# Kernel optimization log

Measured on AMD Instinct MI355X. Metric: run time of the kernel, lower is better.

Reference implementation:

```python
import jax, jax.numpy as jnp
import numpy as np

EPS_NORM = 1e-12   # F.normalize default eps
EPS_COS = 1e-8     # F.cosine_similarity default eps
NUM_LAYERS = 3


def _l2norm(x, eps=EPS_NORM):
    n = jnp.sqrt(jnp.sum(x * x, axis=-1, keepdims=True))
    return x / jnp.maximum(n, eps)


def setup_inputs() -> dict:
    key = jax.random.key(0)
    ks = jax.random.split(key, 16)
    NU, NI, D, E = 200000, 100000, 64, 1000000
    NA, NB, H, F = 20000, 30000, 32, 8
    return {
        "user_emb_w": jax.random.normal(ks[0], (NU, D), jnp.float32) * 0.1,
        "artist_emb_w": jax.random.normal(ks[1], (NA, D), jnp.float32) * 0.1,
        "album_emb_w": jax.random.normal(ks[2], (NB, D), jnp.float32) * 0.1,
        "item_audio": jax.random.normal(ks[3], (NI, D), jnp.float32),
        "adapter_W": jax.random.normal(ks[4], (D, D), jnp.float32) * (1.0 / np.sqrt(D)),
        "adapter_b": jnp.zeros((D,), jnp.float32),
        "mlp_W1": jax.random.normal(ks[5], (H, F), jnp.float32) * (1.0 / np.sqrt(F)),
        "mlp_b1": jnp.zeros((H,), jnp.float32),
        "mlp_W2": jax.random.normal(ks[6], (1, H), jnp.float32) * (1.0 / np.sqrt(H)),
        "mlp_b2": jnp.zeros((1,), jnp.float32),
        "edge_features": jax.random.normal(ks[7], (2 * E, F), jnp.float32),
        "edge_user": jax.random.randint(ks[8], (E,), 0, NU, jnp.int32),
        "edge_item": jax.random.randint(ks[9], (E,), 0, NI, jnp.int32),
        "artist_ids": jax.random.randint(ks[10], (NI,), 0, NA, jnp.int32),
        "album_ids": jax.random.randint(ks[11], (NI,), 0, NB, jnp.int32),
        "user_idx": jax.random.randint(ks[12], (4096,), 0, NU, jnp.int32),
        "pos_item_id": jax.random.randint(ks[13], (4096,), 0, NI, jnp.int32),
    }


def reference(user_emb_w, artist_emb_w, album_emb_w, item_audio,
              adapter_W, adapter_b, mlp_W1, mlp_b1, mlp_W2, mlp_b2,
              edge_features, edge_user, edge_item, artist_ids, album_ids,
              user_idx, pos_item_id):
    NU = user_emb_w.shape[0]
    NI = item_audio.shape[0]
    N = NU + NI

    # EdgeWeightMLP: sigmoid(W2 @ relu(W1 @ f + b1) + b2), per edge -> [2E]
    h = jax.nn.relu(edge_features @ mlp_W1.T + mlp_b1)
    w = jax.nn.sigmoid(h @ mlp_W2.T + mlp_b2)[:, 0]

    # item embedding fusion + AudioAdapter (Linear + L2 normalize)
    item_embed = item_audio + artist_emb_w[artist_ids] + album_emb_w[album_ids]
    item_embed = _l2norm(item_embed @ adapter_W.T + adapter_b)

    x = jnp.concatenate([user_emb_w, item_embed], axis=0)  # [N, D]

    # symmetric edge list in global node ids (items offset by NU)
    item_g = edge_item + NU
    row = jnp.concatenate([edge_user, item_g])   # source
    col = jnp.concatenate([item_g, edge_user])   # target

    # LGConv gcn_norm (no self loops): deg over targets with edge weights
    deg = jax.ops.segment_sum(w, col, num_segments=N)
    dis = jnp.where(deg > 0, jax.lax.rsqrt(jnp.where(deg > 0, deg, 1.0)), 0.0)
    norm_e = dis[row] * w * dis[col]  # [2E]

    for _ in range(NUM_LAYERS):
        msgs = x[row] * norm_e[:, None]              # [2E, D] gather + scale
        x = jax.ops.segment_sum(msgs, col, num_segments=N)  # scatter-add

    x = _l2norm(x)

    u_emb = x[user_idx]                # [B, D]
    pos_emb = x[NU + pos_item_id]      # [B, D]

    # cosine similarity alignment loss (F.cosine_similarity, eps=1e-8)
    un = jnp.sqrt(jnp.sum(u_emb * u_emb, axis=-1))
    pn = jnp.sqrt(jnp.sum(pos_emb * pos_emb, axis=-1))
    cos = jnp.sum(u_emb * pos_emb, axis=-1) / (jnp.maximum(un, EPS_COS) * jnp.maximum(pn, EPS_COS))
    align_loss = jnp.mean(1.0 - cos)

    return u_emb, align_loss
```

## Files before the change

kernel.cpp:

```cpp
#include <hip/hip_runtime.h>
#include <math.h>

#define NU 200000
#define NI 100000
#define NN 300000
#define DD 64
#define EDGES 1000000
#define E2 2000000
#define BATCH 4096
#define SCAN_CHUNK 1024
#define NBLK1 ((NN + SCAN_CHUNK - 1) / SCAN_CHUNK)
#define FIX_SCALE 131072.0f
#define FIX_INV   7.62939453125e-06f

#define MLP_BLOCKS2 ((E2 + 511) / 512)
#define FUSE_BLOCKS4 (NI / 16)
#define COPY_BLOCKS (NU * DD / 4 / 256)
#define PREP_PERIODS 2084
#define PREP_GRID (PREP_PERIODS * 11)

__device__ __forceinline__ unsigned short f2bf(float f) {
    unsigned u = __float_as_uint(f);
    return (unsigned short)((u + 0x7fffu + ((u >> 16) & 1u)) >> 16);
}
__device__ __forceinline__ float bflo(unsigned v) { return __uint_as_float(v << 16); }
__device__ __forceinline__ float bfhi(unsigned v) { return __uint_as_float(v & 0xffff0000u); }

__global__ __launch_bounds__(256) void k_prep(
    const float* __restrict__ ef, const float* __restrict__ W1,
    const float* __restrict__ b1, const float* __restrict__ W2,
    const float* __restrict__ b2, const int* __restrict__ eu,
    const int* __restrict__ ei, float* __restrict__ w,
    unsigned* __restrict__ degc, int* __restrict__ epos,
    const float* __restrict__ item_audio, const float* __restrict__ artist_emb,
    const float* __restrict__ album_emb, const int* __restrict__ artist_ids,
    const int* __restrict__ album_ids, const float* __restrict__ aW,
    const float* __restrict__ ab, const float* __restrict__ user_emb,
    unsigned short* __restrict__ x) {
    __shared__ float4 sW4[64][16];
    __shared__ float4 sv4[16][16];
    __shared__ float4 sW1v[64];
    __shared__ float sb1[32], sW2s[32], sb2v;
    int bid = blockIdx.x;
    int tid = threadIdx.x;
    int r = bid % 11, base = bid / 11;
    if (r < 2) {
        int ablk = base * 2 + r;
        if (ablk >= MLP_BLOCKS2) return;
        if (tid < 64) sW1v[tid] = ((const float4*)W1)[tid];
        else if (tid < 96) sb1[tid - 64] = b1[tid - 64];
        else if (tid < 128) sW2s[tid - 96] = W2[tid - 96];
        else if (tid == 128) sb2v = b2[0];
        __syncthreads();
        int e0 = ablk * 512 + tid;
        int e1 = e0 + 256;
        int e0c = e0 < E2 ? e0 : 0;
        int e1c = e1 < E2 ? e1 : 0;
        int c0 = (e0c < EDGES) ? (NU + ei[e0c]) : eu[e0c - EDGES];
        int c1 = (e1c < EDGES) ? (NU + ei[e1c]) : eu[e1c - EDGES];
        float4 fa0 = ((const float4*)ef)[2 * e0c];
        float4 fa1 = ((const float4*)ef)[2 * e0c + 1];
        float4 fb0 = ((const float4*)ef)[2 * e1c];
        float4 fb1 = ((const float4*)ef)[2 * e1c + 1];
        float z0 = sb2v, z1 = sb2v;
#pragma unroll 8
        for (int i = 0; i < 32; ++i) {
            float4 wa = sW1v[2 * i], wb = sW1v[2 * i + 1];
            float bi = sb1[i], wo = sW2s[i];
            float a0 = bi + fa0.x * wa.x + fa0.y * wa.y + fa0.z * wa.z +
                       fa0.w * wa.w + fa1.x * wb.x + fa1.y * wb.y +
                       fa1.z * wb.z + fa1.w * wb.w;
            float a1 = bi + fb0.x * wa.x + fb0.y * wa.y + fb0.z * wa.z +
                       fb0.w * wa.w + fb1.x * wb.x + fb1.y * wb.y +
                       fb1.z * wb.z + fb1.w * wb.w;
            z0 += wo * fmaxf(a0, 0.0f);
            z1 += wo * fmaxf(a1, 0.0f);
        }
        if (e0 < E2) {
            float we = 1.0f / (1.0f + __expf(-z0));
            w[e0] = we;
            unsigned old = atomicAdd(
                &degc[c0], (1u << 24) | (unsigned)(we * FIX_SCALE + 0.5f));
            epos[e0] = (int)(old >> 24);
        }
        if (e1 < E2) {
            float we = 1.0f / (1.0f + __expf(-z1));
            w[e1] = we;
            unsigned old = atomicAdd(
                &degc[c1], (1u << 24) | (unsigned)(we * FIX_SCALE + 0.5f));
            epos[e1] = (int)(old >> 24);
        }
        return;
    }
    if (r <= 4) {
        int j = base * 3 + (r - 2);
        if (j >= FUSE_BLOCKS4) return;
#pragma unroll
        for (int s = 0; s < 4; ++s) {
            int i4 = tid + s * 256;
            int row = i4 >> 4, c4 = i4 & 15;
            sW4[row][(c4 & 8) | ((c4 ^ row) & 7)] = ((const float4*)aW)[i4];
        }
        __syncthreads();
        int wave = tid >> 6, lane = tid & 63;
        int it0 = j * 16 + wave * 4;
        float* svf = (float*)sv4;
#pragma unroll
        for (int t = 0; t < 4; ++t) {
            int it = it0 + t;
            int ar = artist_ids[it], al = album_ids[it];
            float v = item_audio[it * DD + lane] + artist_emb[ar * DD + lane] +
                      album_emb[al * DD + lane];
            svf[(wave * 4 + t) * DD + lane] = v;
        }
        float bias = ab[lane];
        float t0 = bias, t1 = bias, t2 = bias, t3 = bias;
#pragma unroll
        for (int k4 = 0; k4 < 16; ++k4) {
            float4 wv = sW4[lane][(k4 & 8) | ((k4 ^ lane) & 7)];
            float4 va = sv4[wave * 4 + 0][k4];
            float4 vb = sv4[wave * 4 + 1][k4];
            float4 vc = sv4[wave * 4 + 2][k4];
            float4 vd = sv4[wave * 4 + 3][k4];
            t0 += wv.x * va.x + wv.y * va.y + wv.z * va.z + wv.w * va.w;
            t1 += wv.x * vb.x + wv.y * vb.y + wv.z * vb.z + wv.w * vb.w;
            t2 += wv.x * vc.x + wv.y * vc.y + wv.z * vc.z + wv.w * vc.w;
            t3 += wv.x * vd.x + wv.y * vd.y + wv.z * vd.z + wv.w * vd.w;
        }
        float s0 = t0 * t0, s1 = t1 * t1, s2 = t2 * t2, s3 = t3 * t3;
        for (int m = 32; m >= 1; m >>= 1) {
            s0 += __shfl_xor(s0, m, 64);
            s1 += __shfl_xor(s1, m, 64);
            s2 += __shfl_xor(s2, m, 64);
            s3 += __shfl_xor(s3, m, 64);
        }
        x[(NU + it0 + 0) * DD + lane] = f2bf(t0 / fmaxf(sqrtf(s0), 1e-12f));
        x[(NU + it0 + 1) * DD + lane] = f2bf(t1 / fmaxf(sqrtf(s1), 1e-12f));
        x[(NU + it0 + 2) * DD + lane] = f2bf(t2 / fmaxf(sqrtf(s2), 1e-12f));
        x[(NU + it0 + 3) * DD + lane] = f2bf(t3 / fmaxf(sqrtf(s3), 1e-12f));
        return;
    }
    int cb = base * 6 + (r - 5);
    if (cb >= COPY_BLOCKS) return;
    int i = cb * 256 + tid;
    float4 v = ((const float4*)user_emb)[i];
    ushort4 o;
    o.x = f2bf(v.x); o.y = f2bf(v.y); o.z = f2bf(v.z); o.w = f2bf(v.w);
    ((ushort4*)x)[i] = o;
}

__global__ __launch_bounds__(1024) void k_scan_local(
    const unsigned* __restrict__ degc, int* __restrict__ rowptr,
    int* __restrict__ bsum) {
    __shared__ int sh[SCAN_CHUNK];
    int tid = threadIdx.x;
    int i = blockIdx.x * SCAN_CHUNK + tid;
    int cnt = (i < NN) ? (int)(degc[i] >> 24) : 0;
    int v = (cnt + 7) & ~7;
    sh[tid] = v;
    __syncthreads();
    for (int off = 1; off < SCAN_CHUNK; off <<= 1) {
        int t = (tid >= off) ? sh[tid - off] : 0;
        __syncthreads();
        sh[tid] += t;
        __syncthreads();
    }
    if (i < NN) rowptr[i] = sh[tid] - v;
    if (tid == SCAN_CHUNK - 1) bsum[blockIdx.x] = sh[tid];
}

__global__ __launch_bounds__(512) void k_scan_bsum(int* __restrict__ bsum) {
    __shared__ int sh[512];
    int tid = threadIdx.x;
    int v = (tid < NBLK1) ? bsum[tid] : 0;
    sh[tid] = v;
    __syncthreads();
    for (int off = 1; off < 512; off <<= 1) {
        int t = (tid >= off) ? sh[tid - off] : 0;
        __syncthreads();
        sh[tid] += t;
        __syncthreads();
    }
    if (tid < NBLK1) bsum[tid] = sh[tid] - v;
}

__global__ void k_scan_add_dis(int* __restrict__ rowptr, const int* __restrict__ bsum,
                               const unsigned* __restrict__ degc,
                               float* __restrict__ dis, int2* __restrict__ csre) {
    int i = blockIdx.x * blockDim.x + threadIdx.x;
    if (i >= NN) return;
    int rp = rowptr[i] + bsum[i >> 10];
    rowptr[i] = rp;
    unsigned dc = degc[i];
    int cnt = (int)(dc >> 24);
    int pcnt = (cnt + 7) & ~7;
    float d = (float)(dc & 0xFFFFFFu) * FIX_INV;
    dis[i] = d > 0.0f ? rsqrtf(d) : 0.0f;
    for (int k = cnt; k < pcnt; ++k) csre[rp + k] = make_int2(0, 0);
    if (i == NN - 1) rowptr[NN] = rp + pcnt;
}

__global__ void k_fill(const float* __restrict__ w, const int* __restrict__ eu,
                       const int* __restrict__ ei, const float* __restrict__ dis,
                       const int* __restrict__ rowptr, const int* __restrict__ epos,
                       int2* __restrict__ csre) {
    int e = blockIdx.x * blockDim.x + threadIdx.x;
    if (e >= E2) return;
    int r, c;
    if (e < EDGES) { r = eu[e]; c = NU + ei[e]; }
    else           { r = NU + ei[e - EDGES]; c = eu[e - EDGES]; }
    int pos = rowptr[c] + epos[e];
    csre[pos] = make_int2(r * (DD * 2), __float_as_int(dis[r] * w[e] * dis[c]));
}

__global__ void k_mark(const int* __restrict__ uidx, const int* __restrict__ pidx,
                       const int* __restrict__ rowptr, const int2* __restrict__ csre,
                       unsigned char* __restrict__ flags) {
    int t = blockIdx.x * blockDim.x + threadIdx.x;
    if (t >= 2 * BATCH) return;
    int row = (t < BATCH) ? uidx[t] : NU + pidx[t - BATCH];
    int beg = rowptr[row], end = rowptr[row + 1];
    for (int e = beg; e < end; ++e) flags[((unsigned)csre[e].x) >> 7] = 1;
}

__device__ __forceinline__ void pull4(const char* __restrict__ xb,
                                      const int2* __restrict__ csre,
                                      int beg, int end, int q2, int t8,
                                      float& a0, float& a1, float& a2, float& a3) {
    a0 = a1 = a2 = a3 = 0.0f;
    for (int e = beg; e < end; e += 8) {
        int4 s = *(const int4*)(csre + (e + q2));
        uint2 va = *(const uint2*)(xb + (unsigned)s.x + t8);
        uint2 vb = *(const uint2*)(xb + (unsigned)s.z + t8);
        float wa = __int_as_float(s.y), wb = __int_as_float(s.w);
        a0 = fmaf(bflo(va.x), wa, a0);
        a1 = fmaf(bfhi(va.x), wa, a1);
        a2 = fmaf(bflo(va.y), wa, a2);
        a3 = fmaf(bfhi(va.y), wa, a3);
        a0 = fmaf(bflo(vb.x), wb, a0);
        a1 = fmaf(bfhi(vb.x), wb, a1);
        a2 = fmaf(bflo(vb.y), wb, a2);
        a3 = fmaf(bfhi(vb.y), wb, a3);
    }
    a0 += __shfl_xor(a0, 16, 64); a1 += __shfl_xor(a1, 16, 64);
    a2 += __shfl_xor(a2, 16, 64); a3 += __shfl_xor(a3, 16, 64);
    a0 += __shfl_xor(a0, 32, 64); a1 += __shfl_xor(a1, 32, 64);
    a2 += __shfl_xor(a2, 32, 64); a3 += __shfl_xor(a3, 32, 64);
}

template <bool FLAGS>
__global__ __launch_bounds__(256) void k_prop(
    const unsigned short* __restrict__ x, const int* __restrict__ rowptr,
    const int2* __restrict__ csre, unsigned short* __restrict__ xn,
    const unsigned char* __restrict__ flags) {
    int tid = threadIdx.x;
    int node = blockIdx.x * 4 + (tid >> 6);
    if (node >= NN) return;
    if (FLAGS && !flags[node]) return;
    int lane = tid & 63;
    int q2 = (lane >> 4) << 1;
    int t8 = (lane & 15) * 8;
    float a0, a1, a2, a3;
    pull4((const char*)x, csre, rowptr[node], rowptr[node + 1], q2, t8,
          a0, a1, a2, a3);
    if ((lane >> 4) == 0) {
        unsigned lo = ((unsigned)f2bf(a1) << 16) | (unsigned)f2bf(a0);
        unsigned hi = ((unsigned)f2bf(a3) << 16) | (unsigned)f2bf(a2);
        *(uint2*)((char*)xn + (size_t)node * 128 + t8) = make_uint2(lo, hi);
    }
}

__global__ __launch_bounds__(256) void k_tail(
    const unsigned short* __restrict__ x, const int* __restrict__ rowptr,
    const int2* __restrict__ csre, const int* __restrict__ uidx,
    const int* __restrict__ pidx, float* __restrict__ out) {
    int tid = threadIdx.x;
    int b = blockIdx.x * 4 + (tid >> 6);
    if (b >= BATCH) return;
    int lane = tid & 63;
    int q2 = (lane >> 4) << 1;
    int t8 = (lane & 15) * 8;
    const char* xb = (const char*)x;
    int un = uidx[b], pn = NU + pidx[b];
    float u0, u1, u2, u3, p0, p1, p2, p3, ss, s;
    pull4(xb, csre, rowptr[un], rowptr[un + 1], q2, t8, u0, u1, u2, u3);
    ss = u0 * u0 + u1 * u1 + u2 * u2 + u3 * u3;
    for (int m = 8; m >= 1; m >>= 1) ss += __shfl_xor(ss, m, 64);
    s = 1.0f / fmaxf(sqrtf(ss), 1e-12f);
    u0 *= s; u1 *= s; u2 *= s; u3 *= s;
    pull4(xb, csre, rowptr[pn], rowptr[pn + 1], q2, t8, p0, p1, p2, p3);
    ss = p0 * p0 + p1 * p1 + p2 * p2 + p3 * p3;
    for (int m = 8; m >= 1; m >>= 1) ss += __shfl_xor(ss, m, 64);
    s = 1.0f / fmaxf(sqrtf(ss), 1e-12f);
    p0 *= s; p1 *= s; p2 *= s; p3 *= s;
    if ((lane >> 4) == 0)
        ((float4*)out)[b * 16 + (t8 >> 3)] = make_float4(u0, u1, u2, u3);
    float dot = u0 * p0 + u1 * p1 + u2 * p2 + u3 * p3;
    float uu = u0 * u0 + u1 * u1 + u2 * u2 + u3 * u3;
    float pp = p0 * p0 + p1 * p1 + p2 * p2 + p3 * p3;
    for (int m = 8; m >= 1; m >>= 1) {
        dot += __shfl_xor(dot, m, 64);
        uu  += __shfl_xor(uu, m, 64);
        pp  += __shfl_xor(pp, m, 64);
    }
    if (lane == 0) {
        float cs = dot / (fmaxf(sqrtf(uu), 1e-8f) * fmaxf(sqrtf(pp), 1e-8f));
        atomicAdd(out + BATCH * DD, (1.0f - cs) * (1.0f / BATCH));
    }
}

extern "C" void kernel_launch(void* const* d_in, const int* in_sizes, int n_in,
                              void* d_out, int out_size, void* d_ws, size_t ws_size,
                              hipStream_t stream) {
    const float* user_emb      = (const float*)d_in[0];
    const float* artist_emb    = (const float*)d_in[1];
    const float* album_emb     = (const float*)d_in[2];
    const float* item_audio    = (const float*)d_in[3];
    const float* adapter_W     = (const float*)d_in[4];
    const float* adapter_b     = (const float*)d_in[5];
    const float* mlp_W1        = (const float*)d_in[6];
    const float* mlp_b1        = (const float*)d_in[7];
    const float* mlp_W2        = (const float*)d_in[8];
    const float* mlp_b2        = (const float*)d_in[9];
    const float* edge_features = (const float*)d_in[10];
    const int*   edge_user     = (const int*)d_in[11];
    const int*   edge_item     = (const int*)d_in[12];
    const int*   artist_ids    = (const int*)d_in[13];
    const int*   album_ids     = (const int*)d_in[14];
    const int*   user_idx      = (const int*)d_in[15];
    const int*   pos_item_id   = (const int*)d_in[16];

    char* p = (char*)d_ws;
    unsigned short* XB0 = (unsigned short*)p; p += (size_t)NN * DD * 2;
    unsigned short* XB1 = (unsigned short*)p; p += (size_t)NN * DD * 2;
    float* W       = (float*)p; p += (size_t)E2 * 4;
    int2*  CSRE    = (int2*)p;  p += (size_t)4200000 * 8;
    int*   EPOS    = (int*)p;   p += (size_t)E2 * 4;
    unsigned* DEGC = (unsigned*)p; p += (size_t)NN * 8;
    float* DIS     = (float*)p; p += (size_t)NN * 4;
    int*   ROWPTR  = (int*)p;   p += (size_t)(NN + 1) * 4;
    int*   BSUM    = (int*)p;   p += (size_t)((NBLK1 + 3) & ~3) * 4;
    unsigned char* FLAGS = (unsigned char*)p; p += (size_t)NN;

    hipMemsetAsync(DEGC, 0, NN * sizeof(unsigned), stream);
    hipMemsetAsync(FLAGS, 0, NN, stream);
    hipMemsetAsync((float*)d_out + BATCH * DD, 0, sizeof(float), stream);

    k_prep<<<PREP_GRID, 256, 0, stream>>>(
        edge_features, mlp_W1, mlp_b1, mlp_W2, mlp_b2, edge_user, edge_item,
        W, DEGC, EPOS, item_audio, artist_emb, album_emb, artist_ids, album_ids,
        adapter_W, adapter_b, user_emb, XB0);

    k_scan_local<<<NBLK1, SCAN_CHUNK, 0, stream>>>(DEGC, ROWPTR, BSUM);
    k_scan_bsum<<<1, 512, 0, stream>>>(BSUM);
    k_scan_add_dis<<<(NN + 255) / 256, 256, 0, stream>>>(ROWPTR, BSUM, DEGC, DIS,
                                                         CSRE);
    k_fill<<<(E2 + 255) / 256, 256, 0, stream>>>(W, edge_user, edge_item, DIS,
                                                 ROWPTR, EPOS, CSRE);
    k_mark<<<(2 * BATCH + 255) / 256, 256, 0, stream>>>(user_idx, pos_item_id,
                                                        ROWPTR, CSRE, FLAGS);

    k_prop<false><<<(NN + 3) / 4, 256, 0, stream>>>(XB0, ROWPTR, CSRE, XB1, nullptr);
    k_prop<true><<<(NN + 3) / 4, 256, 0, stream>>>(XB1, ROWPTR, CSRE, XB0, FLAGS);

    k_tail<<<BATCH / 4, 256, 0, stream>>>(XB0, ROWPTR, CSRE, user_idx,
                                          pos_item_id, (float*)d_out);
}
```

Before: 345.1 us.

## Drop CSR padding, factor target norm out of edges, use 16-byte row gathers

Removes the pad-to-8 rows from the CSR edge array and the zero-fill that went with them. The gather loop now bounds-checks each edge slot against the row end instead. The target-side rsqrt degree factor is moved out of each stored edge weight and applied once per node after the reduction; the tail kernel can skip it because L2 normalisation cancels it. The gather is reorganised so 8 lane groups each fetch one edge's 16-byte slice instead of 4 groups fetching two 8-byte slices, trading a per-edge predicate for a smaller edge array and wider loads.

```diff
diff --git a/kernel.cpp b/kernel.cpp
--- a/kernel.cpp
+++ b/kernel.cpp
@@ -155,8 +155,7 @@
     __shared__ int sh[SCAN_CHUNK];
     int tid = threadIdx.x;
     int i = blockIdx.x * SCAN_CHUNK + tid;
-    int cnt = (i < NN) ? (int)(degc[i] >> 24) : 0;
-    int v = (cnt + 7) & ~7;
+    int v = (i < NN) ? (int)(degc[i] >> 24) : 0;
     sh[tid] = v;
     __syncthreads();
     for (int off = 1; off < SCAN_CHUNK; off <<= 1) {
@@ -186,18 +185,15 @@
 
 __global__ void k_scan_add_dis(int* __restrict__ rowptr, const int* __restrict__ bsum,
                                const unsigned* __restrict__ degc,
-                               float* __restrict__ dis, int2* __restrict__ csre) {
+                               float* __restrict__ dis) {
     int i = blockIdx.x * blockDim.x + threadIdx.x;
     if (i >= NN) return;
     int rp = rowptr[i] + bsum[i >> 10];
     rowptr[i] = rp;
     unsigned dc = degc[i];
-    int cnt = (int)(dc >> 24);
-    int pcnt = (cnt + 7) & ~7;
     float d = (float)(dc & 0xFFFFFFu) * FIX_INV;
     dis[i] = d > 0.0f ? rsqrtf(d) : 0.0f;
-    for (int k = cnt; k < pcnt; ++k) csre[rp + k] = make_int2(0, 0);
-    if (i == NN - 1) rowptr[NN] = rp + pcnt;
+    if (i == NN - 1) rowptr[NN] = rp + (int)(dc >> 24);
 }
 
 __global__ void k_fill(const float* __restrict__ w, const int* __restrict__ eu,
@@ -210,7 +206,7 @@
     if (e < EDGES) { r = eu[e]; c = NU + ei[e]; }
     else           { r = NU + ei[e - EDGES]; c = eu[e - EDGES]; }
     int pos = rowptr[c] + epos[e];
-    csre[pos] = make_int2(r * (DD * 2), __float_as_int(dis[r] * w[e] * dis[c]));
+    csre[pos] = make_int2(r * (DD * 2), __float_as_int(dis[r] * w[e]));
 }
 
 __global__ void k_mark(const int* __restrict__ uidx, const int* __restrict__ pidx,
@@ -223,50 +219,53 @@
     for (int e = beg; e < end; ++e) flags[((unsigned)csre[e].x) >> 7] = 1;
 }
 
-__device__ __forceinline__ void pull4(const char* __restrict__ xb,
+__device__ __forceinline__ void pull8(const char* __restrict__ xb,
                                       const int2* __restrict__ csre,
-                                      int beg, int end, int q2, int t8,
-                                      float& a0, float& a1, float& a2, float& a3) {
-    a0 = a1 = a2 = a3 = 0.0f;
+                                      int beg, int end, int g, int t16,
+                                      float (&a)[8]) {
     for (int e = beg; e < end; e += 8) {
-        int4 s = *(const int4*)(csre + (e + q2));
-        uint2 va = *(const uint2*)(xb + (unsigned)s.x + t8);
-        uint2 vb = *(const uint2*)(xb + (unsigned)s.z + t8);
-        float wa = __int_as_float(s.y), wb = __int_as_float(s.w);
-        a0 = fmaf(bflo(va.x), wa, a0);
-        a1 = fmaf(bfhi(va.x), wa, a1);
-        a2 = fmaf(bflo(va.y), wa, a2);
-        a3 = fmaf(bfhi(va.y), wa, a3);
-        a0 = fmaf(bflo(vb.x), wb, a0);
-        a1 = fmaf(bfhi(vb.x), wb, a1);
-        a2 = fmaf(bflo(vb.y), wb, a2);
-        a3 = fmaf(bfhi(vb.y), wb, a3);
-    }
-    a0 += __shfl_xor(a0, 16, 64); a1 += __shfl_xor(a1, 16, 64);
-    a2 += __shfl_xor(a2, 16, 64); a3 += __shfl_xor(a3, 16, 64);
-    a0 += __shfl_xor(a0, 32, 64); a1 += __shfl_xor(a1, 32, 64);
-    a2 += __shfl_xor(a2, 32, 64); a3 += __shfl_xor(a3, 32, 64);
+        int idx = e + g;
+        int2 s = (idx < end) ? csre[idx] : make_int2(0, 0);
+        uint4 v = *(const uint4*)(xb + (unsigned)s.x + t16);
+        float wgt = __int_as_float(s.y);
+        a[0] = fmaf(bflo(v.x), wgt, a[0]);
+        a[1] = fmaf(bfhi(v.x), wgt, a[1]);
+        a[2] = fmaf(bflo(v.y), wgt, a[2]);
+        a[3] = fmaf(bfhi(v.y), wgt, a[3]);
+        a[4] = fmaf(bflo(v.z), wgt, a[4]);
+        a[5] = fmaf(bfhi(v.z), wgt, a[5]);
+        a[6] = fmaf(bflo(v.w), wgt, a[6]);
+        a[7] = fmaf(bfhi(v.w), wgt, a[7]);
+    }
+#pragma unroll
+    for (int m = 8; m <= 32; m <<= 1) {
+#pragma unroll
+        for (int i = 0; i < 8; ++i) a[i] += __shfl_xor(a[i], m, 64);
+    }
 }
 
 template <bool FLAGS>
 __global__ __launch_bounds__(256) void k_prop(
     const unsigned short* __restrict__ x, const int* __restrict__ rowptr,
-    const int2* __restrict__ csre, unsigned short* __restrict__ xn,
-    const unsigned char* __restrict__ flags) {
+    const int2* __restrict__ csre, const float* __restrict__ dis,
+    unsigned short* __restrict__ xn, const unsigned char* __restrict__ flags) {
     int tid = threadIdx.x;
     int node = blockIdx.x * 4 + (tid >> 6);
     if (node >= NN) return;
     if (FLAGS && !flags[node]) return;
     int lane = tid & 63;
-    int q2 = (lane >> 4) << 1;
-    int t8 = (lane & 15) * 8;
-    float a0, a1, a2, a3;
-    pull4((const char*)x, csre, rowptr[node], rowptr[node + 1], q2, t8,
-          a0, a1, a2, a3);
-    if ((lane >> 4) == 0) {
-        unsigned lo = ((unsigned)f2bf(a1) << 16) | (unsigned)f2bf(a0);
-        unsigned hi = ((unsigned)f2bf(a3) << 16) | (unsigned)f2bf(a2);
-        *(uint2*)((char*)xn + (size_t)node * 128 + t8) = make_uint2(lo, hi);
+    int g = lane >> 3;
+    int t16 = (lane & 7) * 16;
+    float a[8] = {0, 0, 0, 0, 0, 0, 0, 0};
+    pull8((const char*)x, csre, rowptr[node], rowptr[node + 1], g, t16, a);
+    float d = dis[node];
+    if (g == 0) {
+        unsigned o0 = ((unsigned)f2bf(a[1] * d) << 16) | (unsigned)f2bf(a[0] * d);
+        unsigned o1 = ((unsigned)f2bf(a[3] * d) << 16) | (unsigned)f2bf(a[2] * d);
+        unsigned o2 = ((unsigned)f2bf(a[5] * d) << 16) | (unsigned)f2bf(a[4] * d);
+        unsigned o3 = ((unsigned)f2bf(a[7] * d) << 16) | (unsigned)f2bf(a[6] * d);
+        *(uint4*)((char*)xn + (size_t)node * 128 + t16) =
+            make_uint4(o0, o1, o2, o3);
     }
 }
 
@@ -278,27 +277,46 @@
     int b = blockIdx.x * 4 + (tid >> 6);
     if (b >= BATCH) return;
     int lane = tid & 63;
-    int q2 = (lane >> 4) << 1;
-    int t8 = (lane & 15) * 8;
+    int g = lane >> 3;
+    int t16 = (lane & 7) * 16;
     const char* xb = (const char*)x;
     int un = uidx[b], pn = NU + pidx[b];
-    float u0, u1, u2, u3, p0, p1, p2, p3, ss, s;
-    pull4(xb, csre, rowptr[un], rowptr[un + 1], q2, t8, u0, u1, u2, u3);
-    ss = u0 * u0 + u1 * u1 + u2 * u2 + u3 * u3;
-    for (int m = 8; m >= 1; m >>= 1) ss += __shfl_xor(ss, m, 64);
+    float u[8] = {0, 0, 0, 0, 0, 0, 0, 0};
+    pull8(xb, csre, rowptr[un], rowptr[un + 1], g, t16, u);
+    float ss = 0.0f;
+#pragma unroll
+    for (int i = 0; i < 8; ++i) ss += u[i] * u[i];
+    ss += __shfl_xor(ss, 1, 64);
+    ss += __shfl_xor(ss, 2, 64);
+    ss += __shfl_xor(ss, 4, 64);
+    float s = 1.0f / fmaxf(sqrtf(ss), 1e-12f);
+#pragma unroll
+    for (int i = 0; i < 8; ++i) u[i] *= s;
+    float p[8] = {0, 0, 0, 0, 0, 0, 0, 0};
+    pull8(xb, csre, rowptr[pn], rowptr[pn + 1], g, t16, p);
+    ss = 0.0f;
+#pragma unroll
+    for (int i = 0; i < 8; ++i) ss += p[i] * p[i];
+    ss += __shfl_xor(ss, 1, 64);
+    ss += __shfl_xor(ss, 2, 64);
+    ss += __shfl_xor(ss, 4, 64);
     s = 1.0f / fmaxf(sqrtf(ss), 1e-12f);
-    u0 *= s; u1 *= s; u2 *= s; u3 *= s;
-    pull4(xb, csre, rowptr[pn], rowptr[pn + 1], q2, t8, p0, p1, p2, p3);
-    ss = p0 * p0 + p1 * p1 + p2 * p2 + p3 * p3;
-    for (int m = 8; m >= 1; m >>= 1) ss += __shfl_xor(ss, m, 64);
-    s = 1.0f / fmaxf(sqrtf(ss), 1e-12f);
-    p0 *= s; p1 *= s; p2 *= s; p3 *= s;
-    if ((lane >> 4) == 0)
-        ((float4*)out)[b * 16 + (t8 >> 3)] = make_float4(u0, u1, u2, u3);
-    float dot = u0 * p0 + u1 * p1 + u2 * p2 + u3 * p3;
-    float uu = u0 * u0 + u1 * u1 + u2 * u2 + u3 * u3;
-    float pp = p0 * p0 + p1 * p1 + p2 * p2 + p3 * p3;
-    for (int m = 8; m >= 1; m >>= 1) {
+#pragma unroll
+    for (int i = 0; i < 8; ++i) p[i] *= s;
+    if (g == 0) {
+        int f4 = b * 16 + (lane & 7) * 2;
+        ((float4*)out)[f4]     = make_float4(u[0], u[1], u[2], u[3]);
+        ((float4*)out)[f4 + 1] = make_float4(u[4], u[5], u[6], u[7]);
+    }
+    float dot = 0.0f, uu = 0.0f, pp = 0.0f;
+#pragma unroll
+    for (int i = 0; i < 8; ++i) {
+        dot += u[i] * p[i];
+        uu += u[i] * u[i];
+        pp += p[i] * p[i];
+    }
+#pragma unroll
+    for (int m = 1; m <= 4; m <<= 1) {
         dot += __shfl_xor(dot, m, 64);
         uu  += __shfl_xor(uu, m, 64);
         pp  += __shfl_xor(pp, m, 64);
@@ -353,15 +371,16 @@
 
     k_scan_local<<<NBLK1, SCAN_CHUNK, 0, stream>>>(DEGC, ROWPTR, BSUM);
     k_scan_bsum<<<1, 512, 0, stream>>>(BSUM);
-    k_scan_add_dis<<<(NN + 255) / 256, 256, 0, stream>>>(ROWPTR, BSUM, DEGC, DIS,
-                                                         CSRE);
+    k_scan_add_dis<<<(NN + 255) / 256, 256, 0, stream>>>(ROWPTR, BSUM, DEGC, DIS);
     k_fill<<<(E2 + 255) / 256, 256, 0, stream>>>(W, edge_user, edge_item, DIS,
                                                  ROWPTR, EPOS, CSRE);
     k_mark<<<(2 * BATCH + 255) / 256, 256, 0, stream>>>(user_idx, pos_item_id,
                                                         ROWPTR, CSRE, FLAGS);
 
-    k_prop<false><<<(NN + 3) / 4, 256, 0, stream>>>(XB0, ROWPTR, CSRE, XB1, nullptr);
-    k_prop<true><<<(NN + 3) / 4, 256, 0, stream>>>(XB1, ROWPTR, CSRE, XB0, FLAGS);
+    k_prop<false><<<(NN + 3) / 4, 256, 0, stream>>>(XB0, ROWPTR, CSRE, DIS, XB1,
+                                                    nullptr);
+    k_prop<true><<<(NN + 3) / 4, 256, 0, stream>>>(XB1, ROWPTR, CSRE, DIS, XB0,
+                                                   FLAGS);
 
     k_tail<<<BATCH / 4, 256, 0, stream>>>(XB0, ROWPTR, CSRE, user_idx,
                                           pos_item_id, (float*)d_out);
```

After: 355.7 us. 3.0% more time.

## Replace three-pass scan with atomic-cursor allocation and fuse marking into propagation

Applied to the files above, without the earlier changes.

The three-kernel prefix scan over padded node degrees becomes a single kernel. Each 1024-node block scans locally and claims its CSR base offset with one atomicAdd on a global cursor, so row segments no longer sit in node order. Row ends now come from the degree count instead of rowptr[node+1], and the target-side dis factor moves out of each edge weight into a per-node scale at output. That scale is a positive constant per row, so it does not change the final L2-normalised tail result. The flag-marking kernel is folded into extra blocks of the first propagation launch, cutting the launch count and the serialised tiny kernels at the cost of a nondeterministic CSR layout.

```diff
diff --git a/kernel.cpp b/kernel.cpp
--- a/kernel.cpp
+++ b/kernel.cpp
@@ -18,6 +18,8 @@
 #define COPY_BLOCKS (NU * DD / 4 / 256)
 #define PREP_PERIODS 2084
 #define PREP_GRID (PREP_PERIODS * 11)
+#define PROP_BLOCKS ((NN + 3) / 4)
+#define MARK_BLOCKS ((2 * BATCH + 255) / 256)
 
 __device__ __forceinline__ unsigned short f2bf(float f) {
     unsigned u = __float_as_uint(f);
@@ -149,13 +151,16 @@
     ((ushort4*)x)[i] = o;
 }
 
-__global__ __launch_bounds__(1024) void k_scan_local(
+__global__ __launch_bounds__(1024) void k_alloc(
     const unsigned* __restrict__ degc, int* __restrict__ rowptr,
-    int* __restrict__ bsum) {
+    float* __restrict__ dis, int2* __restrict__ csre,
+    unsigned* __restrict__ cursor) {
     __shared__ int sh[SCAN_CHUNK];
+    __shared__ int sbase;
     int tid = threadIdx.x;
     int i = blockIdx.x * SCAN_CHUNK + tid;
-    int cnt = (i < NN) ? (int)(degc[i] >> 24) : 0;
+    unsigned dc = (i < NN) ? degc[i] : 0u;
+    int cnt = (int)(dc >> 24);
     int v = (cnt + 7) & ~7;
     sh[tid] = v;
     __syncthreads();
@@ -165,39 +170,16 @@
         sh[tid] += t;
         __syncthreads();
     }
-    if (i < NN) rowptr[i] = sh[tid] - v;
-    if (tid == SCAN_CHUNK - 1) bsum[blockIdx.x] = sh[tid];
-}
-
-__global__ __launch_bounds__(512) void k_scan_bsum(int* __restrict__ bsum) {
-    __shared__ int sh[512];
-    int tid = threadIdx.x;
-    int v = (tid < NBLK1) ? bsum[tid] : 0;
-    sh[tid] = v;
+    if (tid == SCAN_CHUNK - 1)
+        sbase = (int)atomicAdd(cursor, (unsigned)sh[tid]);
     __syncthreads();
-    for (int off = 1; off < 512; off <<= 1) {
-        int t = (tid >= off) ? sh[tid - off] : 0;
-        __syncthreads();
-        sh[tid] += t;
-        __syncthreads();
-    }
-    if (tid < NBLK1) bsum[tid] = sh[tid] - v;
-}
-
-__global__ void k_scan_add_dis(int* __restrict__ rowptr, const int* __restrict__ bsum,
-                               const unsigned* __restrict__ degc,
-                               float* __restrict__ dis, int2* __restrict__ csre) {
-    int i = blockIdx.x * blockDim.x + threadIdx.x;
-    if (i >= NN) return;
-    int rp = rowptr[i] + bsum[i >> 10];
-    rowptr[i] = rp;
-    unsigned dc = degc[i];
-    int cnt = (int)(dc >> 24);
-    int pcnt = (cnt + 7) & ~7;
-    float d = (float)(dc & 0xFFFFFFu) * FIX_INV;
-    dis[i] = d > 0.0f ? rsqrtf(d) : 0.0f;
-    for (int k = cnt; k < pcnt; ++k) csre[rp + k] = make_int2(0, 0);
-    if (i == NN - 1) rowptr[NN] = rp + pcnt;
+    if (i < NN) {
+        int rp = sbase + sh[tid] - v;
+        rowptr[i] = rp;
+        float d = (float)(dc & 0xFFFFFFu) * FIX_INV;
+        dis[i] = d > 0.0f ? rsqrtf(d) : 0.0f;
+        for (int k = cnt; k < v; ++k) csre[rp + k] = make_int2(0, 0);
+    }
 }
 
 __global__ void k_fill(const float* __restrict__ w, const int* __restrict__ eu,
@@ -210,17 +192,7 @@
     if (e < EDGES) { r = eu[e]; c = NU + ei[e]; }
     else           { r = NU + ei[e - EDGES]; c = eu[e - EDGES]; }
     int pos = rowptr[c] + epos[e];
-    csre[pos] = make_int2(r * (DD * 2), __float_as_int(dis[r] * w[e] * dis[c]));
-}
-
-__global__ void k_mark(const int* __restrict__ uidx, const int* __restrict__ pidx,
-                       const int* __restrict__ rowptr, const int2* __restrict__ csre,
-                       unsigned char* __restrict__ flags) {
-    int t = blockIdx.x * blockDim.x + threadIdx.x;
-    if (t >= 2 * BATCH) return;
-    int row = (t < BATCH) ? uidx[t] : NU + pidx[t - BATCH];
-    int beg = rowptr[row], end = rowptr[row + 1];
-    for (int e = beg; e < end; ++e) flags[((unsigned)csre[e].x) >> 7] = 1;
+    csre[pos] = make_int2(r * (DD * 2), __float_as_int(dis[r] * w[e]));
 }
 
 __device__ __forceinline__ void pull4(const char* __restrict__ xb,
@@ -251,29 +223,44 @@
 template <bool FLAGS>
 __global__ __launch_bounds__(256) void k_prop(
     const unsigned short* __restrict__ x, const int* __restrict__ rowptr,
-    const int2* __restrict__ csre, unsigned short* __restrict__ xn,
-    const unsigned char* __restrict__ flags) {
+    const unsigned* __restrict__ degc, const int2* __restrict__ csre,
+    const float* __restrict__ dis, unsigned short* __restrict__ xn,
+    const unsigned char* __restrict__ flags, const int* __restrict__ uidx,
+    const int* __restrict__ pidx, unsigned char* __restrict__ oflags) {
     int tid = threadIdx.x;
+    if (!FLAGS && blockIdx.x >= PROP_BLOCKS) {
+        int t = (blockIdx.x - PROP_BLOCKS) * 256 + tid;
+        if (t >= 2 * BATCH) return;
+        int row = (t < BATCH) ? uidx[t] : NU + pidx[t - BATCH];
+        int beg = rowptr[row];
+        int cnt = (int)(degc[row] >> 24);
+        for (int e = beg; e < beg + cnt; ++e)
+            oflags[((unsigned)csre[e].x) >> 7] = 1;
+        return;
+    }
     int node = blockIdx.x * 4 + (tid >> 6);
     if (node >= NN) return;
     if (FLAGS && !flags[node]) return;
     int lane = tid & 63;
     int q2 = (lane >> 4) << 1;
     int t8 = (lane & 15) * 8;
+    int beg = rowptr[node];
+    int end = beg + (((int)(degc[node] >> 24) + 7) & ~7);
     float a0, a1, a2, a3;
-    pull4((const char*)x, csre, rowptr[node], rowptr[node + 1], q2, t8,
-          a0, a1, a2, a3);
+    pull4((const char*)x, csre, beg, end, q2, t8, a0, a1, a2, a3);
+    float d = dis[node];
     if ((lane >> 4) == 0) {
-        unsigned lo = ((unsigned)f2bf(a1) << 16) | (unsigned)f2bf(a0);
-        unsigned hi = ((unsigned)f2bf(a3) << 16) | (unsigned)f2bf(a2);
+        unsigned lo = ((unsigned)f2bf(a1 * d) << 16) | (unsigned)f2bf(a0 * d);
+        unsigned hi = ((unsigned)f2bf(a3 * d) << 16) | (unsigned)f2bf(a2 * d);
         *(uint2*)((char*)xn + (size_t)node * 128 + t8) = make_uint2(lo, hi);
     }
 }
 
 __global__ __launch_bounds__(256) void k_tail(
     const unsigned short* __restrict__ x, const int* __restrict__ rowptr,
-    const int2* __restrict__ csre, const int* __restrict__ uidx,
-    const int* __restrict__ pidx, float* __restrict__ out) {
+    const unsigned* __restrict__ degc, const int2* __restrict__ csre,
+    const int* __restrict__ uidx, const int* __restrict__ pidx,
+    float* __restrict__ out) {
     int tid = threadIdx.x;
     int b = blockIdx.x * 4 + (tid >> 6);
     if (b >= BATCH) return;
@@ -282,13 +269,15 @@
     int t8 = (lane & 15) * 8;
     const char* xb = (const char*)x;
     int un = uidx[b], pn = NU + pidx[b];
+    int ub = rowptr[un], ue = ub + (((int)(degc[un] >> 24) + 7) & ~7);
+    int pb = rowptr[pn], pe = pb + (((int)(degc[pn] >> 24) + 7) & ~7);
     float u0, u1, u2, u3, p0, p1, p2, p3, ss, s;
-    pull4(xb, csre, rowptr[un], rowptr[un + 1], q2, t8, u0, u1, u2, u3);
+    pull4(xb, csre, ub, ue, q2, t8, u0, u1, u2, u3);
     ss = u0 * u0 + u1 * u1 + u2 * u2 + u3 * u3;
     for (int m = 8; m >= 1; m >>= 1) ss += __shfl_xor(ss, m, 64);
     s = 1.0f / fmaxf(sqrtf(ss), 1e-12f);
     u0 *= s; u1 *= s; u2 *= s; u3 *= s;
-    pull4(xb, csre, rowptr[pn], rowptr[pn + 1], q2, t8, p0, p1, p2, p3);
+    pull4(xb, csre, pb, pe, q2, t8, p0, p1, p2, p3);
     ss = p0 * p0 + p1 * p1 + p2 * p2 + p3 * p3;
     for (int m = 8; m >= 1; m >>= 1) ss += __shfl_xor(ss, m, 64);
     s = 1.0f / fmaxf(sqrtf(ss), 1e-12f);
@@ -339,10 +328,10 @@
     unsigned* DEGC = (unsigned*)p; p += (size_t)NN * 8;
     float* DIS     = (float*)p; p += (size_t)NN * 4;
     int*   ROWPTR  = (int*)p;   p += (size_t)(NN + 1) * 4;
-    int*   BSUM    = (int*)p;   p += (size_t)((NBLK1 + 3) & ~3) * 4;
     unsigned char* FLAGS = (unsigned char*)p; p += (size_t)NN;
-
-    hipMemsetAsync(DEGC, 0, NN * sizeof(unsigned), stream);
+    unsigned* CURSOR = DEGC + NN;
+
+    hipMemsetAsync(DEGC, 0, (NN + 1) * sizeof(unsigned), stream);
     hipMemsetAsync(FLAGS, 0, NN, stream);
     hipMemsetAsync((float*)d_out + BATCH * DD, 0, sizeof(float), stream);
 
@@ -351,18 +340,16 @@
         W, DEGC, EPOS, item_audio, artist_emb, album_emb, artist_ids, album_ids,
         adapter_W, adapter_b, user_emb, XB0);
 
-    k_scan_local<<<NBLK1, SCAN_CHUNK, 0, stream>>>(DEGC, ROWPTR, BSUM);
-    k_scan_bsum<<<1, 512, 0, stream>>>(BSUM);
-    k_scan_add_dis<<<(NN + 255) / 256, 256, 0, stream>>>(ROWPTR, BSUM, DEGC, DIS,
-                                                         CSRE);
+    k_alloc<<<NBLK1, SCAN_CHUNK, 0, stream>>>(DEGC, ROWPTR, DIS, CSRE, CURSOR);
     k_fill<<<(E2 + 255) / 256, 256, 0, stream>>>(W, edge_user, edge_item, DIS,
                                                  ROWPTR, EPOS, CSRE);
-    k_mark<<<(2 * BATCH + 255) / 256, 256, 0, stream>>>(user_idx, pos_item_id,
-                                                        ROWPTR, CSRE, FLAGS);
-
-    k_prop<false><<<(NN + 3) / 4, 256, 0, stream>>>(XB0, ROWPTR, CSRE, XB1, nullptr);
-    k_prop<true><<<(NN + 3) / 4, 256, 0, stream>>>(XB1, ROWPTR, CSRE, XB0, FLAGS);
-
-    k_tail<<<BATCH / 4, 256, 0, stream>>>(XB0, ROWPTR, CSRE, user_idx,
+
+    k_prop<false><<<PROP_BLOCKS + MARK_BLOCKS, 256, 0, stream>>>(
+        XB0, ROWPTR, DEGC, CSRE, DIS, XB1, nullptr, user_idx, pos_item_id,
+        FLAGS);
+    k_prop<true><<<PROP_BLOCKS, 256, 0, stream>>>(
+        XB1, ROWPTR, DEGC, CSRE, DIS, XB0, FLAGS, nullptr, nullptr, nullptr);
+
+    k_tail<<<BATCH / 4, 256, 0, stream>>>(XB0, ROWPTR, DEGC, CSRE, user_idx,
                                           pos_item_id, (float*)d_out);
 }
```

Result: slower. 360.3 us (+4.4%).
